# Optimization experiments

Hardware: AMD Instinct MI355X
Metric: run time of the kernel (lower is better)

The kernel has to match this reference:

```python
import jax, jax.numpy as jnp
import numpy as np

V, E, H = 32000, 512, 1024
B, T = 32, 48
PAD = 0


def setup_inputs() -> dict:
    key = jax.random.key(0)
    ks = jax.random.split(key, 9)
    s = 0.05
    emb = jax.random.normal(ks[0], (V, E), jnp.float32) * s
    emb = emb.at[PAD].set(0.0)  # padding_idx row is zero in nn.Embedding
    return {
        "initial_hidden_state": jax.random.normal(ks[1], (B, H), jnp.float32),
        "target_sequence": jax.random.randint(ks[2], (B, T), 0, V),
        "emb": emb,
        "W_ih": jax.random.normal(ks[3], (3 * H, E), jnp.float32) * s,  # [r;z;n] input weights
        "W_hh": jax.random.normal(ks[4], (3 * H, H), jnp.float32) * s,
        "b_ih": jax.random.normal(ks[5], (3 * H,), jnp.float32) * s,
        "b_hh": jax.random.normal(ks[6], (3 * H,), jnp.float32) * s,
        "W_cls": jax.random.normal(ks[7], (V, H), jnp.float32) * s,
        "b_cls": jax.random.normal(ks[8], (V,), jnp.float32) * s,
    }


def _decode(initial_hidden_state, target_sequence, emb, W_ih, W_hh, b_ih, b_hh, W_cls, b_cls):
    # teacher forcing: sample_probability = 0.0 -> use_sample False
    idx_t = target_sequence.T  # [T, B]

    def step(h, y_idx):
        x = emb[y_idx]                                 # [B, E] embedding gather
        gi = x @ W_ih.T + b_ih                         # [B, 3H]
        gh = h @ W_hh.T + b_hh                         # [B, 3H]
        i_r, i_z, i_n = jnp.split(gi, 3, axis=-1)
        h_r, h_z, h_n = jnp.split(gh, 3, axis=-1)
        r = jax.nn.sigmoid(i_r + h_r)
        z = jax.nn.sigmoid(i_z + h_z)
        n = jnp.tanh(i_n + r * h_n)
        h_new = (1.0 - z) * n + z * h                  # torch GRUCell update
        score = h_new @ W_cls.T + b_cls                # [B, V]
        return h_new, score

    _, scores = jax.lax.scan(step, initial_hidden_state, idx_t)  # [T, B, V]
    return jnp.transpose(scores, (1, 0, 2))                      # [B, T, V]


def reference(initial_hidden_state, target_sequence, emb, W_ih, W_hh, b_ih, b_hh, W_cls, b_cls):
    return _decode(initial_hidden_state, target_sequence, emb, W_ih, W_hh, b_ih, b_hh, W_cls, b_cls)
```

## Files before the change

### kernel.cpp

```cpp
#include <hip/hip_runtime.h>
#include <hip/hip_bf16.h>

typedef __attribute__((ext_vector_type(8))) short short8;
typedef __attribute__((ext_vector_type(4))) float f32x4;
typedef __attribute__((ext_vector_type(4))) unsigned int u32x4;

#define T_STEPS 48
#define BATCH 32
#define EDIM 512
#define HDIM 1024
#define VOCAB 32000
#define GRU_BLOCKS 64
#define JPB 16
#define SENT 0x7FFF7FFFu
#define N_TILES 750
#define CNT_STRIDE 16
#define EARLY_WORKERS 128

#define HS_T_STRIDE 16384

__device__ __forceinline__ unsigned short f2bf(float f) {
    __hip_bfloat16 h = __float2bfloat16(f);
    return *reinterpret_cast<unsigned short*>(&h);
}
__device__ __forceinline__ float bf2f(unsigned short u) {
    union { unsigned int i; float f; } v;
    v.i = ((unsigned int)u) << 16;
    return v.f;
}

typedef __attribute__((address_space(1))) const void GAS;
typedef __attribute__((address_space(3))) void LAS;
__device__ __forceinline__ void gload_lds16(const unsigned short* g, unsigned short* l) {
    __builtin_amdgcn_global_load_lds((GAS*)g, (LAS*)(unsigned)(uintptr_t)l, 16, 0, 0);
}

__device__ __forceinline__ void store16_coh(unsigned int* p, u32x4 v) {
    asm volatile("global_store_dwordx4 %0, %1, off sc0 sc1"
                 :: "v"((unsigned long long)(uintptr_t)p), "v"(v) : "memory");
}

__global__ __launch_bounds__(256) void prep_kernel(
    const float* __restrict__ h0, const int* __restrict__ tseq,
    const float* __restrict__ emb, const float* __restrict__ w_ih,
    const float* __restrict__ w_hh, const float* __restrict__ w_cls,
    unsigned short* __restrict__ wcls_bf, unsigned short* __restrict__ wih_bf,
    unsigned short* __restrict__ whh_bf, unsigned short* __restrict__ x_bf,
    unsigned int* __restrict__ hs32, unsigned int* __restrict__ cnt8)
{
    const long R0 = (long)VOCAB * HDIM / 4;
    const long R1 = (long)3 * HDIM * EDIM / 4;
    const long R2 = (long)3 * HDIM * HDIM / 4;
    const long R3 = (long)T_STEPS * BATCH * EDIM / 4;
    const long R4 = (long)HS_T_STRIDE;
    const long R5 = (long)T_STEPS * HS_T_STRIDE / 4;
    const long R6 = 512;
    const long total = R0 + R1 + R2 + R3 + R4 + R5 + R6;

    for (long i = (long)blockIdx.x * blockDim.x + threadIdx.x; i < total;
         i += (long)gridDim.x * blockDim.x) {
        if (i < R0) {
            float4 v = reinterpret_cast<const float4*>(w_cls)[i];
            ushort4 u = { f2bf(v.x), f2bf(v.y), f2bf(v.z), f2bf(v.w) };
            *reinterpret_cast<ushort4*>(wcls_bf + i * 4) = u;
        } else if (i < R0 + R1) {
            long j = i - R0;
            float4 v = reinterpret_cast<const float4*>(w_ih)[j];
            ushort4 u = { f2bf(v.x), f2bf(v.y), f2bf(v.z), f2bf(v.w) };
            *reinterpret_cast<ushort4*>(wih_bf + j * 4) = u;
        } else if (i < R0 + R1 + R2) {
            long j = i - R0 - R1;
            float4 v = reinterpret_cast<const float4*>(w_hh)[j];
            ushort4 u = { f2bf(v.x), f2bf(v.y), f2bf(v.z), f2bf(v.w) };
            *reinterpret_cast<ushort4*>(whh_bf + j * 4) = u;
        } else if (i < R0 + R1 + R2 + R3) {
            long j = i - R0 - R1 - R2;
            int m = (int)(j >> 7);
            int kk4 = (int)(j & 127);
            int t = m >> 5, b = m & 31;
            int tok = tseq[b * T_STEPS + t];
            float4 v = reinterpret_cast<const float4*>(emb)[(long)tok * (EDIM / 4) + kk4];
            ushort4 u = { f2bf(v.x), f2bf(v.y), f2bf(v.z), f2bf(v.w) };
            *reinterpret_cast<ushort4*>(x_bf + (long)m * EDIM + kk4 * 4) = u;
        } else if (i < R0 + R1 + R2 + R3 + R4) {
            long j = i - R0 - R1 - R2 - R3;
            int w = (int)(j >> 5), b = (int)(j & 31);
            unsigned short a = f2bf(h0[b * HDIM + 2 * w]);
            unsigned short c = f2bf(h0[b * HDIM + 2 * w + 1]);
            hs32[j] = (unsigned)a | ((unsigned)c << 16);
        } else if (i < R0 + R1 + R2 + R3 + R4 + R5) {
            long j = i - R0 - R1 - R2 - R3 - R4;
            uint4 s = { SENT, SENT, SENT, SENT };
            reinterpret_cast<uint4*>(hs32 + HS_T_STRIDE)[j] = s;
        } else {
            long j = i - R0 - R1 - R2 - R3 - R4 - R5;
            uint4 z = { 0u, 0u, 0u, 0u };
            reinterpret_cast<uint4*>(cnt8)[j] = z;
        }
    }
}

__global__ __launch_bounds__(256) void gemm_gi(
    const unsigned short* __restrict__ A, const unsigned short* __restrict__ B,
    const float* __restrict__ bias, float* __restrict__ C, int K, int Ntot, int nM)
{
    const int nwg = gridDim.x;
    const int lin = blockIdx.x;
    const int q = nwg >> 3;
    const int wg = (lin & 7) * q + (lin >> 3);
    const int mi = wg % nM, ni = wg / nM;
    const int m0 = mi * 128, n0 = ni * 128;

    const int tid = threadIdx.x;
    const int lane = tid & 63;
    const int wid = tid >> 6;
    const int wr = wid >> 1, wc = wid & 1;

    __shared__ __align__(16) unsigned short As[128 * 32];
    __shared__ __align__(16) unsigned short Bs[128 * 32];

    f32x4 acc[4][4] = {};
    const int NT = K >> 5;
    const int srow = (lane >> 2);
    const int skk = (lane & 3) * 8;

    for (int kt = 0; kt < NT; ++kt) {
        __syncthreads();
        {
            const int kb = kt * 32;
#pragma unroll
            for (int h2 = 0; h2 < 2; ++h2) {
                const int i = wid + h2 * 4;
                const int row = i * 16 + srow;
                gload_lds16(A + (size_t)(m0 + row) * K + kb + skk, As + i * 512);
                gload_lds16(B + (size_t)(n0 + row) * K + kb + skk, Bs + i * 512);
            }
        }
        __syncthreads();

        const int kg = lane >> 4;
        const int l15 = lane & 15;
        short8 af[4], bf[4];
#pragma unroll
        for (int i = 0; i < 4; ++i) {
            af[i] = *(const short8*)(As + ((wr * 64 + i * 16 + l15) * 32 + kg * 8));
            bf[i] = *(const short8*)(Bs + ((wc * 64 + i * 16 + l15) * 32 + kg * 8));
        }
#pragma unroll
        for (int i = 0; i < 4; ++i)
#pragma unroll
            for (int j = 0; j < 4; ++j)
                acc[i][j] = __builtin_amdgcn_mfma_f32_16x16x32_bf16(af[i], bf[j], acc[i][j], 0, 0, 0);
    }

    const int l15 = lane & 15, lhi = lane >> 4;
#pragma unroll
    for (int i = 0; i < 4; ++i)
#pragma unroll
        for (int j = 0; j < 4; ++j) {
            int col = n0 + wc * 64 + j * 16 + l15;
            float bv = bias[col];
#pragma unroll
            for (int q2 = 0; q2 < 4; ++q2) {
                int row = m0 + wr * 64 + i * 16 + lhi * 4 + q2;
                C[(size_t)row * Ntot + col] = acc[i][j][q2] + bv;
            }
        }
}

__global__ __launch_bounds__(512, 1) void fused_kernel(
    unsigned int* __restrict__ hs32, unsigned int* __restrict__ hrow32,
    const unsigned short* __restrict__ whh_bf,
    const float* __restrict__ gi, const float* __restrict__ b_hh,
    const float* __restrict__ h0,
    const unsigned short* __restrict__ wcls_bf, const float* __restrict__ b_cls,
    float* __restrict__ out, unsigned int* __restrict__ cnt8,
    unsigned int* __restrict__ tileq)
{
    __shared__ __align__(16) char smem[124160];
    __shared__ unsigned short Hs[BATCH][JPB];
    __shared__ int sTile;

    const int tid = threadIdx.x;
    const int bid = blockIdx.x;
    const int lane = tid & 63, wid = tid >> 6;
    const int l15 = lane & 15, kg = lane >> 4;

    if (bid < GRU_BLOCKS) {
        unsigned short (*Wl)[1032] = reinterpret_cast<unsigned short (*)[1032]>(smem);
        float (*P)[32][49] = reinterpret_cast<float (*)[32][49]>(smem + 99072);

        const int j0 = bid * JPB;
        for (int c = tid; c < 48 * 128; c += 512) {
            int row = c >> 7, k8 = (c & 127) * 8;
            int g = row >> 4, jj = row & 15;
            *(short8*)&Wl[row][k8] =
                *(const short8*)(whh_bf + (size_t)(g * HDIM + j0 + jj) * HDIM + k8);
        }
        const int b = tid >> 4, jj = tid & 15;
        const int gj = j0 + jj;
        const float bhr = b_hh[gj];
        const float bhz = b_hh[HDIM + gj];
        const float bhn = b_hh[2 * HDIM + gj];
        float hloc = h0[b * HDIM + gj];
        __syncthreads();

        for (int t = 0; t < T_STEPS; ++t) {
            const size_t tb = (size_t)t * HS_T_STRIDE;
            const float* gr = gi + (size_t)(t * BATCH + b) * (3 * HDIM);
            float xr = gr[gj], xz = gr[HDIM + gj], xn = gr[2 * HDIM + gj];

            if (t) {
                if (wid == 0) {
                    const unsigned int* cp = cnt8 + (size_t)t * CNT_STRIDE;
                    for (;;) {
                        unsigned v = (lane < 8)
                            ? __hip_atomic_load(cp + lane, __ATOMIC_RELAXED, __HIP_MEMORY_SCOPE_AGENT)
                            : 8u;
                        if (__all(v >= 8u)) break;
                        __builtin_amdgcn_s_sleep(2);
                    }
                }
                __syncthreads();
                asm volatile("" ::: "memory");
            }

            if (tid < 256) {
                const int kq = wid * 256;
                unsigned wv[8][8];
#pragma unroll
                for (int ks = 0; ks < 8; ++ks) {
                    const int wbase = wid * 128 + ks * 16 + kg * 4;
#pragma unroll
                    for (int mi2 = 0; mi2 < 2; ++mi2) {
                        const int bb = mi2 * 16 + l15;
#pragma unroll
                        for (int q = 0; q < 4; ++q)
                            wv[ks][mi2 * 4 + q] = *(const unsigned*)(
                                hs32 + tb + (size_t)(wbase + q) * 32 + bb);
                    }
                }
                for (;;) {
                    int bad = 0;
#pragma unroll
                    for (int ks = 0; ks < 8; ++ks)
#pragma unroll
                        for (int i = 0; i < 8; ++i)
                            bad |= (wv[ks][i] == SENT);
                    if (!__any(bad)) break;
                    __builtin_amdgcn_s_sleep(1);
#pragma unroll
                    for (int ks = 0; ks < 8; ++ks)
#pragma unroll
                        for (int i = 0; i < 8; ++i)
                            if (wv[ks][i] == SENT) {
                                const int mi2 = i >> 2, q = i & 3;
                                wv[ks][i] = __hip_atomic_load(
                                    hs32 + tb + (size_t)(wid * 128 + ks * 16 + kg * 4 + q) * 32 + (mi2 * 16 + l15),
                                    __ATOMIC_RELAXED, __HIP_MEMORY_SCOPE_AGENT);
                            }
                }
                f32x4 acc[2][3] = {};
#pragma unroll
                for (int ks = 0; ks < 8; ++ks) {
                    const int kb = kq + ks * 32 + kg * 8;
                    union U8 { unsigned u[4]; short8 s; };
                    short8 ah[2];
#pragma unroll
                    for (int mi2 = 0; mi2 < 2; ++mi2) {
                        U8 x;
#pragma unroll
                        for (int q = 0; q < 4; ++q) x.u[q] = wv[ks][mi2 * 4 + q];
                        ah[mi2] = x.s;
                    }
#pragma unroll
                    for (int fr = 0; fr < 3; ++fr) {
                        short8 bh = *(const short8*)&Wl[fr * 16 + l15][kb];
#pragma unroll
                        for (int mi2 = 0; mi2 < 2; ++mi2)
                            acc[mi2][fr] = __builtin_amdgcn_mfma_f32_16x16x32_bf16(ah[mi2], bh, acc[mi2][fr], 0, 0, 0);
                    }
                }
#pragma unroll
                for (int mi2 = 0; mi2 < 2; ++mi2)
#pragma unroll
                    for (int fr = 0; fr < 3; ++fr)
#pragma unroll
                        for (int q = 0; q < 4; ++q)
                            P[wid][mi2 * 16 + kg * 4 + q][fr * 16 + l15] = acc[mi2][fr][q];
            }
            __syncthreads();

            {
                float ghr = 0.f, ghz = 0.f, ghn = 0.f;
#pragma unroll
                for (int w = 0; w < 4; ++w) {
                    ghr += P[w][b][jj];
                    ghz += P[w][b][16 + jj];
                    ghn += P[w][b][32 + jj];
                }
                float r = 1.f / (1.f + __expf(-(xr + ghr + bhr)));
                float z = 1.f / (1.f + __expf(-(xz + ghz + bhz)));
                float n = tanhf(xn + r * (ghn + bhn));
                float hnew = (1.f - z) * n + z * hloc;
                hloc = hnew;
                Hs[b][jj] = f2bf(hnew);
            }
            __syncthreads();

            if (tid < 64) {
                const int q = tid >> 3, c = tid & 7;
                u32x4 d;
#pragma unroll
                for (int w2 = 0; w2 < 4; ++w2) {
                    int bb = c * 4 + w2;
                    d[w2] = (unsigned)Hs[bb][2 * q] | ((unsigned)Hs[bb][2 * q + 1] << 16);
                }
                store16_coh(hs32 + (size_t)(t + 1) * HS_T_STRIDE + (size_t)((j0 >> 1) + q) * 32 + c * 4, d);
            } else if (tid < 128) {
                const int i = tid - 64, bb = i >> 1, half = i & 1;
                u32x4 d;
#pragma unroll
                for (int w2 = 0; w2 < 4; ++w2) {
                    int q = half * 4 + w2;
                    d[w2] = (unsigned)Hs[bb][2 * q] | ((unsigned)Hs[bb][2 * q + 1] << 16);
                }
                store16_coh(hrow32 + ((size_t)t * BATCH + bb) * 512 + (j0 >> 1) + half * 4, d);
            }
            __syncthreads();
            if (tid == 0)
                __hip_atomic_fetch_add(cnt8 + (size_t)(t + 1) * CNT_STRIDE + (bid & 7), 1u,
                                       __ATOMIC_RELAXED, __HIP_MEMORY_SCOPE_AGENT);
        }
    } else if (bid >= GRU_BLOCKS + EARLY_WORKERS) {
        if (wid == 0) {
            const unsigned int* cp = cnt8 + (size_t)T_STEPS * CNT_STRIDE;
            for (;;) {
                unsigned v = (lane < 8)
                    ? __hip_atomic_load(cp + lane, __ATOMIC_RELAXED, __HIP_MEMORY_SCOPE_AGENT)
                    : 8u;
                if (__all(v >= 8u)) break;
                __builtin_amdgcn_s_sleep(64);
            }
        }
        __syncthreads();
    }

    const unsigned short* hrowA = (const unsigned short*)hrow32;
    const int srow = lane >> 2;
    const int skk = (lane & 3) * 8;
    const int wm = wid >> 1, wn = wid & 1;

    unsigned short* As0 = (unsigned short*)(smem);
    unsigned short* Bs0 = (unsigned short*)(smem + 16384);
    unsigned short* As1 = (unsigned short*)(smem + 32768);
    unsigned short* Bs1 = (unsigned short*)(smem + 49152);

    for (;;) {
        __syncthreads();
        if (tid == 0)
            sTile = (int)__hip_atomic_fetch_add(tileq, 1u, __ATOMIC_RELAXED, __HIP_MEMORY_SCOPE_AGENT);
        __syncthreads();
        const int k = sTile;
        if (k >= N_TILES) break;
        const int mi = k / 125, ni = k - mi * 125;
        const int m0 = mi * 256, n0 = ni * 256;

        {
            if (wid == 0) {
                const unsigned int* cp = cnt8 + (size_t)(mi * 8 + 8) * CNT_STRIDE;
                for (;;) {
                    unsigned v = (lane < 8)
                        ? __hip_atomic_load(cp + lane, __ATOMIC_RELAXED, __HIP_MEMORY_SCOPE_AGENT)
                        : 8u;
                    if (__all(v >= 8u)) break;
                    __builtin_amdgcn_s_sleep(32);
                }
            }
            __syncthreads();
            asm volatile("" ::: "memory");
        }

        f32x4 acc[4][8] = {};

#define STAGE(KT, AB, BB)                                                      \
        {                                                                      \
            const int kb = (KT) * 32;                                          \
            _Pragma("unroll")                                                  \
            for (int h2 = 0; h2 < 2; ++h2) {                                   \
                const int i = wid + h2 * 8;                                    \
                const int row = i * 16 + srow;                                 \
                gload_lds16(hrowA + (size_t)(m0 + row) * HDIM + kb + skk, (AB) + i * 512); \
                gload_lds16(wcls_bf + (size_t)(n0 + row) * HDIM + kb + skk, (BB) + i * 512); \
            }                                                                  \
        }
#define COMPUTE(AB, BB)                                                        \
        {                                                                      \
            short8 af[4], bf[8];                                               \
            _Pragma("unroll")                                                  \
            for (int i = 0; i < 4; ++i)                                        \
                af[i] = *(const short8*)((AB) + ((wm * 64 + i * 16 + l15) * 32 + kg * 8)); \
            _Pragma("unroll")                                                  \
            for (int j = 0; j < 8; ++j)                                        \
                bf[j] = *(const short8*)((BB) + ((wn * 128 + j * 16 + l15) * 32 + kg * 8)); \
            _Pragma("unroll")                                                  \
            for (int i = 0; i < 4; ++i)                                        \
                _Pragma("unroll")                                              \
                for (int j = 0; j < 8; ++j)                                    \
                    acc[i][j] = __builtin_amdgcn_mfma_f32_16x16x32_bf16(af[i], bf[j], acc[i][j], 0, 0, 0); \
        }

        STAGE(0, As0, Bs0);
        __syncthreads();
        for (int it = 0; it < 16; ++it) {
            const int kt0 = 2 * it;
            STAGE(kt0 + 1, As1, Bs1);
            COMPUTE(As0, Bs0);
            __syncthreads();
            if (kt0 + 2 < 32) STAGE(kt0 + 2, As0, Bs0);
            COMPUTE(As1, Bs1);
            __syncthreads();
        }
#undef STAGE
#undef COMPUTE

        const int lhi = lane >> 4;
#pragma unroll
        for (int i = 0; i < 4; ++i)
#pragma unroll
            for (int j = 0; j < 8; ++j) {
                int col = n0 + wn * 128 + j * 16 + l15;
                float bv = b_cls[col];
#pragma unroll
                for (int q2 = 0; q2 < 4; ++q2) {
                    int row = m0 + wm * 64 + i * 16 + lhi * 4 + q2;
                    int t = row >> 5, bb = row & 31;
                    __builtin_nontemporal_store(acc[i][j][q2] + bv,
                        &out[(size_t)(bb * T_STEPS + t) * VOCAB + col]);
                }
            }
    }
}

extern "C" void kernel_launch(void* const* d_in, const int* in_sizes, int n_in,
                              void* d_out, int out_size, void* d_ws, size_t ws_size,
                              hipStream_t stream) {
    const float* h0    = (const float*)d_in[0];
    const int*   tseq  = (const int*)d_in[1];
    const float* emb   = (const float*)d_in[2];
    const float* w_ih  = (const float*)d_in[3];
    const float* w_hh  = (const float*)d_in[4];
    const float* b_ih  = (const float*)d_in[5];
    const float* b_hh  = (const float*)d_in[6];
    const float* w_cls = (const float*)d_in[7];
    const float* b_cls = (const float*)d_in[8];
    float* out = (float*)d_out;

    char* w = (char*)d_ws;
    unsigned short* wcls_bf = (unsigned short*)w; w += (size_t)VOCAB * HDIM * 2;
    unsigned short* wih_bf  = (unsigned short*)w; w += (size_t)3 * HDIM * EDIM * 2;
    unsigned short* whh_bf  = (unsigned short*)w; w += (size_t)3 * HDIM * HDIM * 2;
    unsigned short* x_bf    = (unsigned short*)w; w += (size_t)T_STEPS * BATCH * EDIM * 2;
    unsigned int*   hs32    = (unsigned int*)w;   w += (size_t)(T_STEPS + 1) * HS_T_STRIDE * 4;
    unsigned int*   hrow32  = (unsigned int*)w;   w += (size_t)T_STEPS * BATCH * 512 * 4;
    float* gi               = (float*)w;          w += (size_t)T_STEPS * BATCH * 3 * HDIM * 4;
    unsigned int* cnt8      = (unsigned int*)w;   w += 8192;
    unsigned int* tileq     = cnt8 + 1024;

    prep_kernel<<<2048, 256, 0, stream>>>(h0, tseq, emb, w_ih, w_hh, w_cls,
                                          wcls_bf, wih_bf, whh_bf, x_bf, hs32, cnt8);

    gemm_gi<<<(T_STEPS * BATCH / 128) * (3 * HDIM / 128), 256, 0, stream>>>(
        x_bf, wih_bf, b_ih, gi, EDIM, 3 * HDIM, T_STEPS * BATCH / 128);

    fused_kernel<<<256, 512, 0, stream>>>(hs32, hrow32, whh_bf, gi, b_hh, h0,
                                          wcls_bf, b_cls, out, cnt8, tileq);
}
```

Baseline: 345.4 us.

## Fold input-gate GEMM into fused kernel with per-timestep readiness counters

Removes the separate gemm_gi launch and has 64 worker blocks inside the persistent fused kernel compute the input-gate projection tiles through an atomic tile queue. Each finished tile bumps a per-128-row counter, and GRU blocks wait on that counter before reading gi for a timestep, so the recurrence can start before the whole projection is done. Gi values are written and read with relaxed atomics to keep them coherent across blocks. The cost is fewer early classifier workers and an added spin-wait in the recurrent loop, and the change relies on the cnt8 region past offset 1280 being zeroed by prep.

```diff
diff --git a/kernel.cpp b/kernel.cpp
--- a/kernel.cpp
+++ b/kernel.cpp
@@ -14,8 +14,9 @@
 #define JPB 16
 #define SENT 0x7FFF7FFFu
 #define N_TILES 750
+#define GI_TILES 288
 #define CNT_STRIDE 16
-#define EARLY_WORKERS 128
+#define EARLY_WORKERS 64
 
 #define HS_T_STRIDE 16384
 
@@ -27,6 +28,14 @@
     union { unsigned int i; float f; } v;
     v.i = ((unsigned int)u) << 16;
     return v.f;
+}
+__device__ __forceinline__ float aloadf(const float* p) {
+    unsigned u = __hip_atomic_load((const unsigned*)p, __ATOMIC_RELAXED, __HIP_MEMORY_SCOPE_AGENT);
+    union { unsigned u; float f; } c; c.u = u; return c.f;
+}
+__device__ __forceinline__ void astoref(float* p, float v) {
+    union { float f; unsigned u; } c; c.f = v;
+    __hip_atomic_store((unsigned*)p, c.u, __ATOMIC_RELAXED, __HIP_MEMORY_SCOPE_AGENT);
 }
 
 typedef __attribute__((address_space(1))) const void GAS;
@@ -100,82 +109,16 @@
     }
 }
 
-__global__ __launch_bounds__(256) void gemm_gi(
-    const unsigned short* __restrict__ A, const unsigned short* __restrict__ B,
-    const float* __restrict__ bias, float* __restrict__ C, int K, int Ntot, int nM)
-{
-    const int nwg = gridDim.x;
-    const int lin = blockIdx.x;
-    const int q = nwg >> 3;
-    const int wg = (lin & 7) * q + (lin >> 3);
-    const int mi = wg % nM, ni = wg / nM;
-    const int m0 = mi * 128, n0 = ni * 128;
-
-    const int tid = threadIdx.x;
-    const int lane = tid & 63;
-    const int wid = tid >> 6;
-    const int wr = wid >> 1, wc = wid & 1;
-
-    __shared__ __align__(16) unsigned short As[128 * 32];
-    __shared__ __align__(16) unsigned short Bs[128 * 32];
-
-    f32x4 acc[4][4] = {};
-    const int NT = K >> 5;
-    const int srow = (lane >> 2);
-    const int skk = (lane & 3) * 8;
-
-    for (int kt = 0; kt < NT; ++kt) {
-        __syncthreads();
-        {
-            const int kb = kt * 32;
-#pragma unroll
-            for (int h2 = 0; h2 < 2; ++h2) {
-                const int i = wid + h2 * 4;
-                const int row = i * 16 + srow;
-                gload_lds16(A + (size_t)(m0 + row) * K + kb + skk, As + i * 512);
-                gload_lds16(B + (size_t)(n0 + row) * K + kb + skk, Bs + i * 512);
-            }
-        }
-        __syncthreads();
-
-        const int kg = lane >> 4;
-        const int l15 = lane & 15;
-        short8 af[4], bf[4];
-#pragma unroll
-        for (int i = 0; i < 4; ++i) {
-            af[i] = *(const short8*)(As + ((wr * 64 + i * 16 + l15) * 32 + kg * 8));
-            bf[i] = *(const short8*)(Bs + ((wc * 64 + i * 16 + l15) * 32 + kg * 8));
-        }
-#pragma unroll
-        for (int i = 0; i < 4; ++i)
-#pragma unroll
-            for (int j = 0; j < 4; ++j)
-                acc[i][j] = __builtin_amdgcn_mfma_f32_16x16x32_bf16(af[i], bf[j], acc[i][j], 0, 0, 0);
-    }
-
-    const int l15 = lane & 15, lhi = lane >> 4;
-#pragma unroll
-    for (int i = 0; i < 4; ++i)
-#pragma unroll
-        for (int j = 0; j < 4; ++j) {
-            int col = n0 + wc * 64 + j * 16 + l15;
-            float bv = bias[col];
-#pragma unroll
-            for (int q2 = 0; q2 < 4; ++q2) {
-                int row = m0 + wr * 64 + i * 16 + lhi * 4 + q2;
-                C[(size_t)row * Ntot + col] = acc[i][j][q2] + bv;
-            }
-        }
-}
 
 __global__ __launch_bounds__(512, 1) void fused_kernel(
     unsigned int* __restrict__ hs32, unsigned int* __restrict__ hrow32,
     const unsigned short* __restrict__ whh_bf,
-    const float* __restrict__ gi, const float* __restrict__ b_hh,
+    float* __restrict__ gi, const float* __restrict__ b_hh,
     const float* __restrict__ h0,
     const unsigned short* __restrict__ wcls_bf, const float* __restrict__ b_cls,
-    float* __restrict__ out, unsigned int* __restrict__ cnt8,
-    unsigned int* __restrict__ tileq)
+    const unsigned short* __restrict__ x_bf, const unsigned short* __restrict__ wih_bf,
+    const float* __restrict__ b_ih,
+    float* __restrict__ out, unsigned int* __restrict__ cnt8)
 {
     __shared__ __align__(16) char smem[124160];
     __shared__ unsigned short Hs[BATCH][JPB];
@@ -185,6 +128,9 @@
     const int bid = blockIdx.x;
     const int lane = tid & 63, wid = tid >> 6;
     const int l15 = lane & 15, kg = lane >> 4;
+
+    unsigned int* tileq   = cnt8 + 1024;
+    unsigned int* giTileq = cnt8 + 1040;
 
     if (bid < GRU_BLOCKS) {
         unsigned short (*Wl)[1032] = reinterpret_cast<unsigned short (*)[1032]>(smem);
@@ -207,23 +153,26 @@
 
         for (int t = 0; t < T_STEPS; ++t) {
             const size_t tb = (size_t)t * HS_T_STRIDE;
+
+            {
+                const unsigned int* cp = cnt8 + (size_t)t * CNT_STRIDE;
+                const unsigned int* gq = cnt8 + 1280 + (size_t)(t >> 2) * CNT_STRIDE;
+                for (;;) {
+                    unsigned ok;
+                    if (lane < 8)
+                        ok = t ? (__hip_atomic_load(cp + lane, __ATOMIC_RELAXED, __HIP_MEMORY_SCOPE_AGENT) >= 8u) : 1u;
+                    else if (lane == 8)
+                        ok = (__hip_atomic_load(gq, __ATOMIC_RELAXED, __HIP_MEMORY_SCOPE_AGENT) >= 24u) ? 1u : 0u;
+                    else
+                        ok = 1u;
+                    if (__all(ok != 0u)) break;
+                    __builtin_amdgcn_s_sleep(2);
+                }
+                asm volatile("" ::: "memory");
+            }
+
             const float* gr = gi + (size_t)(t * BATCH + b) * (3 * HDIM);
-            float xr = gr[gj], xz = gr[HDIM + gj], xn = gr[2 * HDIM + gj];
-
-            if (t) {
-                if (wid == 0) {
-                    const unsigned int* cp = cnt8 + (size_t)t * CNT_STRIDE;
-                    for (;;) {
-                        unsigned v = (lane < 8)
-                            ? __hip_atomic_load(cp + lane, __ATOMIC_RELAXED, __HIP_MEMORY_SCOPE_AGENT)
-                            : 8u;
-                        if (__all(v >= 8u)) break;
-                        __builtin_amdgcn_s_sleep(2);
-                    }
-                }
-                __syncthreads();
-                asm volatile("" ::: "memory");
-            }
+            float xr = aloadf(gr + gj), xz = aloadf(gr + HDIM + gj), xn = aloadf(gr + 2 * HDIM + gj);
 
             if (tid < 256) {
                 const int kq = wid * 256;
@@ -332,7 +281,64 @@
                 __hip_atomic_fetch_add(cnt8 + (size_t)(t + 1) * CNT_STRIDE + (bid & 7), 1u,
                                        __ATOMIC_RELAXED, __HIP_MEMORY_SCOPE_AGENT);
         }
-    } else if (bid >= GRU_BLOCKS + EARLY_WORKERS) {
+    } else if (bid < GRU_BLOCKS + EARLY_WORKERS) {
+        unsigned short* As0 = (unsigned short*)(smem);
+        unsigned short* Bs0 = (unsigned short*)(smem + 16384);
+        const int srow = lane >> 2, skk = (lane & 3) * 8;
+        const int wr2 = wid >> 2, wc2 = wid & 3;
+        const int lhi = lane >> 4;
+
+        for (;;) {
+            __syncthreads();
+            if (tid == 0)
+                sTile = (int)__hip_atomic_fetch_add(giTileq, 1u, __ATOMIC_RELAXED, __HIP_MEMORY_SCOPE_AGENT);
+            __syncthreads();
+            const int k = sTile;
+            if (k >= GI_TILES) break;
+            const int mi = k / 24, ni = k - mi * 24;
+            const int m0 = mi * 128, n0 = ni * 128;
+
+            f32x4 acc[4][2] = {};
+            for (int kt = 0; kt < 16; ++kt) {
+                __syncthreads();
+                {
+                    const int kb = kt * 32;
+                    const int row = wid * 16 + srow;
+                    gload_lds16(x_bf + (size_t)(m0 + row) * EDIM + kb + skk, As0 + wid * 512);
+                    gload_lds16(wih_bf + (size_t)(n0 + row) * EDIM + kb + skk, Bs0 + wid * 512);
+                }
+                __syncthreads();
+                short8 af[4], bfr[2];
+#pragma unroll
+                for (int i = 0; i < 4; ++i)
+                    af[i] = *(const short8*)(As0 + ((wr2 * 64 + i * 16 + l15) * 32 + kg * 8));
+#pragma unroll
+                for (int j = 0; j < 2; ++j)
+                    bfr[j] = *(const short8*)(Bs0 + ((wc2 * 32 + j * 16 + l15) * 32 + kg * 8));
+#pragma unroll
+                for (int i = 0; i < 4; ++i)
+#pragma unroll
+                    for (int j = 0; j < 2; ++j)
+                        acc[i][j] = __builtin_amdgcn_mfma_f32_16x16x32_bf16(af[i], bfr[j], acc[i][j], 0, 0, 0);
+            }
+#pragma unroll
+            for (int i = 0; i < 4; ++i)
+#pragma unroll
+                for (int j = 0; j < 2; ++j) {
+                    int col = n0 + wc2 * 32 + j * 16 + l15;
+                    float bv = b_ih[col];
+#pragma unroll
+                    for (int q2 = 0; q2 < 4; ++q2) {
+                        int row = m0 + wr2 * 64 + i * 16 + lhi * 4 + q2;
+                        astoref(&gi[(size_t)row * (3 * HDIM) + col], acc[i][j][q2] + bv);
+                    }
+                }
+            __syncthreads();
+            if (tid == 0)
+                __hip_atomic_fetch_add(cnt8 + 1280 + (size_t)mi * CNT_STRIDE, 1u,
+                                       __ATOMIC_RELAXED, __HIP_MEMORY_SCOPE_AGENT);
+        }
+    } else {
         if (wid == 0) {
             const unsigned int* cp = cnt8 + (size_t)T_STEPS * CNT_STRIDE;
             for (;;) {
@@ -396,18 +402,18 @@
         }
 #define COMPUTE(AB, BB)                                                        \
         {                                                                      \
-            short8 af[4], bf[8];                                               \
+            short8 af[4], bfr[8];                                              \
             _Pragma("unroll")                                                  \
             for (int i = 0; i < 4; ++i)                                        \
                 af[i] = *(const short8*)((AB) + ((wm * 64 + i * 16 + l15) * 32 + kg * 8)); \
             _Pragma("unroll")                                                  \
             for (int j = 0; j < 8; ++j)                                        \
-                bf[j] = *(const short8*)((BB) + ((wn * 128 + j * 16 + l15) * 32 + kg * 8)); \
+                bfr[j] = *(const short8*)((BB) + ((wn * 128 + j * 16 + l15) * 32 + kg * 8)); \
             _Pragma("unroll")                                                  \
             for (int i = 0; i < 4; ++i)                                        \
                 _Pragma("unroll")                                              \
                 for (int j = 0; j < 8; ++j)                                    \
-                    acc[i][j] = __builtin_amdgcn_mfma_f32_16x16x32_bf16(af[i], bf[j], acc[i][j], 0, 0, 0); \
+                    acc[i][j] = __builtin_amdgcn_mfma_f32_16x16x32_bf16(af[i], bfr[j], acc[i][j], 0, 0, 0); \
         }
 
         STAGE(0, As0, Bs0);
@@ -465,14 +471,11 @@
     unsigned int*   hrow32  = (unsigned int*)w;   w += (size_t)T_STEPS * BATCH * 512 * 4;
     float* gi               = (float*)w;          w += (size_t)T_STEPS * BATCH * 3 * HDIM * 4;
     unsigned int* cnt8      = (unsigned int*)w;   w += 8192;
-    unsigned int* tileq     = cnt8 + 1024;
 
     prep_kernel<<<2048, 256, 0, stream>>>(h0, tseq, emb, w_ih, w_hh, w_cls,
                                           wcls_bf, wih_bf, whh_bf, x_bf, hs32, cnt8);
 
-    gemm_gi<<<(T_STEPS * BATCH / 128) * (3 * HDIM / 128), 256, 0, stream>>>(
-        x_bf, wih_bf, b_ih, gi, EDIM, 3 * HDIM, T_STEPS * BATCH / 128);
-
     fused_kernel<<<256, 512, 0, stream>>>(hs32, hrow32, whh_bf, gi, b_hh, h0,
-                                          wcls_bf, b_cls, out, cnt8, tileq);
-}
+                                          wcls_bf, b_cls, x_bf, wih_bf, b_ih,
+                                          out, cnt8);
+}
```

Result: slower. 358.2 us (+3.7%).
